# Kernel tuning notes

Measured on AMD Instinct MI355X. Metric: run time of the kernel, lower is better.

Reference implementation:

```python
import jax, jax.numpy as jnp
import numpy as np

B, S, F, L = 128, 512, 128, 1024  # batch, seq_len, n_features, latent_dim


def _gru_step(h, x, W_ih, W_hh, b_ih, b_hh):
    # PyTorch GRUCell math, gate order (r, z, n)
    gi = x @ W_ih.T + b_ih            # [B, 3L]
    gh = h @ W_hh.T + b_hh            # [B, 3L]
    ir, iz, inn = jnp.split(gi, 3, axis=-1)
    hr, hz, hn = jnp.split(gh, 3, axis=-1)
    r = jax.nn.sigmoid(ir + hr)
    z = jax.nn.sigmoid(iz + hz)
    n = jnp.tanh(inn + r * hn)
    return (1.0 - z) * n + z * h


def setup_inputs() -> dict:
    key = jax.random.key(0)
    ks = jax.random.split(key, 12)
    s_e = 1.0 / np.sqrt(L)
    u = lambda k, shape: jax.random.uniform(k, shape, jnp.float32, -s_e, s_e)
    return {
        "x": jax.random.normal(ks[0], (B, S, F), jnp.float32),
        # encoder GRU (single layer)
        "W_ih_e": u(ks[1], (3 * L, F)),
        "W_hh_e": u(ks[2], (3 * L, L)),
        "b_ih_e": u(ks[3], (3 * L,)),
        "b_hh_e": u(ks[4], (3 * L,)),
        # decoder GRUCell
        "W_ih_d": u(ks[5], (3 * L, F)),
        "W_hh_d": u(ks[6], (3 * L, L)),
        "b_ih_d": u(ks[7], (3 * L,)),
        "b_hh_d": u(ks[8], (3 * L,)),
        # decoder Linear(latent_dim -> n_features)
        "W_out": u(ks[9], (F, L)),
        "b_out": u(ks[10], (F,)),
    }


def reference(x, W_ih_e, W_hh_e, b_ih_e, b_hh_e,
              W_ih_d, W_hh_d, b_ih_d, b_hh_d, W_out, b_out):
    seq_len = x.shape[1]

    # ---- encoder: GRU over time, return final hidden state h_n [B, L] ----
    def enc_step(h, x_t):
        h = _gru_step(h, x_t, W_ih_e, W_hh_e, b_ih_e, b_hh_e)
        return h, None

    h0 = jnp.zeros((x.shape[0], W_hh_e.shape[1]), x.dtype)
    h_n, _ = jax.lax.scan(enc_step, h0, jnp.swapaxes(x, 0, 1))  # scan over [S,B,F]

    # ---- decoder: GRUCell + Linear unrolled seq_len steps ----
    x_init = h_n @ W_out.T + b_out  # [B, F]

    def dec_step(carry, _):
        h, x_i = carry
        h = _gru_step(h, x_i, W_ih_d, W_hh_d, b_ih_d, b_hh_d)
        x_i = h @ W_out.T + b_out
        return (h, x_i), x_i

    _, xs = jax.lax.scan(dec_step, (h_n, x_init), None, length=seq_len)  # [S,B,F]
    out = jnp.swapaxes(xs, 0, 1)  # [B,S,F]
    return jnp.flip(out, axis=1)
```

## Files before the change

kernel.cpp:

```cpp
#include <hip/hip_runtime.h>
#include <hip/hip_bf16.h>


#define B_ 128
#define S_ 512
#define F_ 128
#define L_ 1024
#define U_ 8
#define NWG_E 128
#define NWG_D 144

typedef __bf16 bf16x8 __attribute__((ext_vector_type(8)));
typedef float  f32x4  __attribute__((ext_vector_type(4)));
typedef float  f32x16 __attribute__((ext_vector_type(16)));
typedef int    i32x4  __attribute__((ext_vector_type(4)));
typedef unsigned long long u64;

union pk2 { unsigned u; __bf16 h[2]; };
union fu  { float f; unsigned u; };

#define MFMA32(a, b, c) __builtin_amdgcn_mfma_f32_32x32x16_bf16(a, b, c, 0, 0, 0)
#define Z16 f32x16{0.f,0.f,0.f,0.f,0.f,0.f,0.f,0.f,0.f,0.f,0.f,0.f,0.f,0.f,0.f,0.f}

#define LDG16(dst, p) asm volatile("global_load_dwordx4 %0, %1, off sc0 sc1" : "=v"(dst) : "v"(p))
#define VMWAIT16(a) asm volatile("s_waitcnt vmcnt(0)" \
    : "+v"(a[0]),"+v"(a[1]),"+v"(a[2]),"+v"(a[3]),"+v"(a[4]),"+v"(a[5]),"+v"(a[6]),"+v"(a[7]), \
      "+v"(a[8]),"+v"(a[9]),"+v"(a[10]),"+v"(a[11]),"+v"(a[12]),"+v"(a[13]),"+v"(a[14]),"+v"(a[15]) \
    :: "memory")
#define SB0() __builtin_amdgcn_sched_barrier(0)

#define O_H0   0
#define O_H1   (256*1024)
#define O_H32  (512*1024)
#define O_CTR  (1024*1024)
#define O_ZERO_END (1024*1024 + 8192)
#define O_XB   O_ZERO_END
#define O_WEH  (O_XB  + 16777216)
#define O_WEX  (O_WEH + 8388608)
#define O_BE   (O_WEX + 1048576)
#define O_WD   (O_BE  + 16384)
#define O_BD   (O_WD  + 8388608)
#define O_WC   (O_BD  + 16384)
#define O_WOB  (O_WC  + 6291456)


__global__ void k_xcvt(const float* __restrict__ x, __bf16* __restrict__ xb, int n) {
    int i = blockIdx.x * 256 + threadIdx.x;
    int stride = gridDim.x * 256;
    for (; i < n; i += stride) xb[i] = (__bf16)x[i];
}

__global__ void k_woutb(const float* __restrict__ Wout, __bf16* __restrict__ Wob, int n) {
    int i = blockIdx.x * 256 + threadIdx.x;
    if (i < n) Wob[i] = (__bf16)Wout[i];
}

__global__ void k_pack_enc(const float* __restrict__ Wih, const float* __restrict__ Whh,
                           const float* __restrict__ bih, const float* __restrict__ bhh,
                           __bf16* __restrict__ Weh, __bf16* __restrict__ Wex,
                           float* __restrict__ be) {
    int g = blockIdx.x, tid = threadIdx.x;
    for (int i = tid; i < 32 * 1024; i += 256) {
        int c = i >> 10, k = i & 1023;
        int u = g * U_ + (c >> 2), gate = c & 3;
        float v = 0.f;
        if (gate == 0)      v = Whh[(size_t)u * 1024 + k];
        else if (gate == 1) v = Whh[(size_t)(1024 + u) * 1024 + k];
        else if (gate == 3) v = Whh[(size_t)(2048 + u) * 1024 + k];
        Weh[((size_t)g * 32 + c) * 1024 + k] = (__bf16)v;
    }
    for (int i = tid; i < 32 * 128; i += 256) {
        int c = i >> 7, k = i & 127;
        int u = g * U_ + (c >> 2), gate = c & 3;
        float v = 0.f;
        if (gate == 0)      v = Wih[(size_t)u * 128 + k];
        else if (gate == 1) v = Wih[(size_t)(1024 + u) * 128 + k];
        else if (gate == 2) v = Wih[(size_t)(2048 + u) * 128 + k];
        Wex[((size_t)g * 32 + c) * 128 + k] = (__bf16)v;
    }
    if (tid < 32) {
        int c = tid, u = g * U_ + (c >> 2), gate = c & 3;
        float v;
        if (gate == 0)      v = bih[u] + bhh[u];
        else if (gate == 1) v = bih[1024 + u] + bhh[1024 + u];
        else if (gate == 2) v = bih[2048 + u];
        else                v = bhh[2048 + u];
        be[g * 32 + c] = v;
    }
}

__global__ void k_wcomb(const float* __restrict__ Wihd, const float* __restrict__ Wout,
                        __bf16* __restrict__ Wc) {
    __shared__ float a[8][128];
    int r0 = blockIdx.x * 8, tid = threadIdx.x;
    for (int i = tid; i < 8 * 128; i += 256)
        a[i >> 7][i & 127] = Wihd[(size_t)(r0 + (i >> 7)) * 128 + (i & 127)];
    __syncthreads();
    for (int j = tid; j < 1024; j += 256) {
        float acc[8] = {0, 0, 0, 0, 0, 0, 0, 0};
        for (int f = 0; f < 128; ++f) {
            float w = Wout[(size_t)f * 1024 + j];
#pragma unroll
            for (int r = 0; r < 8; ++r) acc[r] += a[r][f] * w;
        }
        for (int r = 0; r < 8; ++r) Wc[(size_t)(r0 + r) * 1024 + j] = (__bf16)acc[r];
    }
}

__global__ void k_pack_dec(const float* __restrict__ Whhd, const __bf16* __restrict__ Wc,
                           const float* __restrict__ Wihd,
                           const float* __restrict__ bihd, const float* __restrict__ bhhd,
                           const float* __restrict__ bout,
                           __bf16* __restrict__ Wd, float* __restrict__ bd) {
    int g = blockIdx.x, tid = threadIdx.x;
    for (int i = tid; i < 32 * 1024; i += 256) {
        int c = i >> 10, k = i & 1023;
        int u = g * U_ + (c >> 2), gate = c & 3;
        float v;
        if (gate == 0)      v = Whhd[(size_t)u * 1024 + k] + (float)Wc[(size_t)u * 1024 + k];
        else if (gate == 1) v = Whhd[(size_t)(1024 + u) * 1024 + k] + (float)Wc[(size_t)(1024 + u) * 1024 + k];
        else if (gate == 2) v = (float)Wc[(size_t)(2048 + u) * 1024 + k];
        else                v = Whhd[(size_t)(2048 + u) * 1024 + k];
        Wd[((size_t)g * 32 + c) * 1024 + k] = (__bf16)v;
    }
    if (tid < 32) {
        int c = tid;
        int u = g * U_ + (c >> 2), gate = c & 3;
        int row = (gate == 0) ? u : (gate == 1) ? (1024 + u) : (2048 + u);
        float v;
        if (gate <= 1) {
            float d = 0.f;
            for (int f = 0; f < 128; ++f) d += Wihd[(size_t)row * 128 + f] * bout[f];
            v = d + bihd[row] + bhhd[row];
        } else if (gate == 2) {
            float d = 0.f;
            for (int f = 0; f < 128; ++f) d += Wihd[(size_t)row * 128 + f] * bout[f];
            v = d + bihd[row];
        } else {
            v = bhhd[row];
        }
        bd[g * 32 + c] = v;
    }
}


__device__ __forceinline__ void bar_arrive(unsigned* base, int g) {
    if (threadIdx.x == 0)
        __hip_atomic_fetch_add(base + (g & 15) * 32, 1u,
                               __ATOMIC_RELAXED, __HIP_MEMORY_SCOPE_AGENT);
}

__device__ __forceinline__ void bar_wait(unsigned* base, unsigned tgt) {
    if (threadIdx.x == 0) {
        for (;;) {
            unsigned sum = 0;
#pragma unroll
            for (int j = 0; j < 16; ++j)
                sum += __hip_atomic_load(base + j * 32, __ATOMIC_RELAXED, __HIP_MEMORY_SCOPE_AGENT);
            if (sum >= tgt) break;
            __builtin_amdgcn_s_sleep(1);
        }
    }
    __syncthreads();
}

__global__ __launch_bounds__(512, 2) void k_enc(
    const __bf16* __restrict__ xb, const __bf16* __restrict__ Weh,
    const __bf16* __restrict__ Wex, const float* __restrict__ be,
    __bf16* __restrict__ h0, __bf16* __restrict__ h1,
    float* __restrict__ h32, unsigned* __restrict__ ctr) {
    __shared__ __align__(16) __bf16 sWh[32][1032];
    __shared__ __align__(16) __bf16 sWx[32][136];
    __shared__ float sB[32];
    __shared__ __align__(16) float sGa[128][36];
    __shared__ __align__(16) float sGb[128][36];
    const int g = blockIdx.x, tid = threadIdx.x;
    const int lane = tid & 63, wave = tid >> 6;

    for (int i = tid; i < 32 * 128; i += 512) {
        int c = i >> 7, k8 = i & 127;
        *(i32x4*)&sWh[c][k8 * 8] = *(const i32x4*)(Weh + ((size_t)g * 32 + c) * 1024 + k8 * 8);
    }
    for (int i = tid; i < 32 * 16; i += 512) {
        int c = i >> 4, k8 = i & 15;
        *(i32x4*)&sWx[c][k8 * 8] = *(const i32x4*)(Wex + ((size_t)g * 32 + c) * 128 + k8 * 8);
    }
    if (tid < 32) sB[tid] = be[g * 32 + tid];
    __syncthreads();

    const int bcol = lane & 31;
    const int koff = (lane >> 5) * 8;
    const int mrow = (wave & 3) * 32 + bcol;
    const int kb = (wave >> 2) * 32;
    const bool up = (wave >= 4);

    bf16x8 xrg[8];
    if (up) {
#pragma unroll
        for (int kt = 0; kt < 8; ++kt) xrg[kt] = *(const bf16x8*)(&sWx[bcol][kt * 16 + koff]);
    }

    const int erow = tid >> 2, pair = tid & 3;
    const int hidx2 = g * 512 + erow * 4 + pair;
    float ha = 0.f, hb = 0.f;

    f32x16 accx = Z16;
    if (up) {
        const __bf16* xr = xb + (size_t)mrow * 65536;
#pragma unroll
        for (int kt = 0; kt < 8; ++kt)
            accx = MFMA32(*(const bf16x8*)(xr + kt * 16 + koff), xrg[kt], accx);
    }

    for (int s = 0; s < 512; ++s) {
        const __bf16* hcur = (s & 1) ? h1 : h0;
        __bf16* hnxt = (s & 1) ? h0 : h1;
        {
            f32x16 aA = up ? accx : Z16;
            f32x16 aB = Z16;
            const __bf16* hr = hcur + ((size_t)(kb * 2 + (koff >> 3)) << 10) + mrow * 8;
            bf16x8 af[16];
#pragma unroll
            for (int i = 0; i < 16; ++i) LDG16(af[i], hr + i * 2048);
            VMWAIT16(af); SB0();
#pragma unroll
            for (int i = 0; i < 16; ++i) {
                const bf16x8 b = *(const bf16x8*)(&sWh[bcol][(kb + i) * 16 + koff]);
                if (i & 1) aB = MFMA32(af[i], b, aB); else aA = MFMA32(af[i], b, aA);
                LDG16(af[i], hr + (16 + i) * 2048);
            }
            VMWAIT16(af); SB0();
#pragma unroll
            for (int i = 0; i < 16; ++i) {
                const bf16x8 b = *(const bf16x8*)(&sWh[bcol][(kb + 16 + i) * 16 + koff]);
                if (i & 1) aB = MFMA32(af[i], b, aB); else aA = MFMA32(af[i], b, aA);
            }
            f32x16 acc = aA + aB;
            int rb = (wave & 3) * 32 + 4 * (lane >> 5);
            float (*sg)[36] = up ? sGb : sGa;
#pragma unroll
            for (int r = 0; r < 16; ++r)
                sg[rb + (r & 3) + 8 * (r >> 2)][bcol] = acc[r];
        }
        __syncthreads();
        {
            f32x4 g0 = *(const f32x4*)&sGa[erow][pair * 8] + *(const f32x4*)&sGb[erow][pair * 8];
            f32x4 g1 = *(const f32x4*)&sGa[erow][pair * 8 + 4] + *(const f32x4*)&sGb[erow][pair * 8 + 4];
            int c0 = pair * 8;
            float r = 1.f / (1.f + __expf(-(g0[0] + sB[c0 + 0])));
            float z = 1.f / (1.f + __expf(-(g0[1] + sB[c0 + 1])));
            float n = tanhf(g0[2] + sB[c0 + 2] + r * (g0[3] + sB[c0 + 3]));
            ha = (1.f - z) * n + z * ha;
            r = 1.f / (1.f + __expf(-(g1[0] + sB[c0 + 4])));
            z = 1.f / (1.f + __expf(-(g1[1] + sB[c0 + 5])));
            n = tanhf(g1[2] + sB[c0 + 6] + r * (g1[3] + sB[c0 + 7]));
            hb = (1.f - z) * n + z * hb;
            pk2 p; p.h[0] = (__bf16)ha; p.h[1] = (__bf16)hb;
            __hip_atomic_store((unsigned*)hnxt + hidx2, p.u, __ATOMIC_RELAXED, __HIP_MEMORY_SCOPE_AGENT);
            if (s == 511) {
                h32[erow * 1024 + g * 8 + pair * 2]     = ha;
                h32[erow * 1024 + g * 8 + pair * 2 + 1] = hb;
            }
        }
        if (s < 511) {
            __syncthreads();
            bar_arrive(ctr, g);
            if (up) {
                f32x16 ax = Z16;
                const __bf16* xr = xb + (size_t)mrow * 65536 + (size_t)(s + 1) * 128;
#pragma unroll
                for (int kt = 0; kt < 8; ++kt)
                    ax = MFMA32(*(const bf16x8*)(xr + kt * 16 + koff), xrg[kt], ax);
                accx = ax;
            }
            bar_wait(ctr, (unsigned)(s + 1) * NWG_E);
        }
    }
}

__global__ __launch_bounds__(512, 2) void k_dec(
    const __bf16* __restrict__ Wd, const float* __restrict__ bd,
    const __bf16* __restrict__ Wob, const float* __restrict__ bout,
    __bf16* __restrict__ h0, __bf16* __restrict__ h1,
    const float* __restrict__ h32, float* __restrict__ out,
    unsigned* __restrict__ ctr) {
    __shared__ __align__(16) __bf16 sW[32][1032];
    __shared__ float sB[32];
    __shared__ __align__(16) float sGa[128][36];
    __shared__ __align__(16) float sGb[128][36];
    const int g = blockIdx.x, tid = threadIdx.x;
    const int lane = tid & 63, wave = tid >> 6;
    const bool gwg = (g < 128);
    const int go = g - 128;

    if (gwg) {
        for (int i = tid; i < 32 * 128; i += 512) {
            int c = i >> 7, k8 = i & 127;
            *(i32x4*)&sW[c][k8 * 8] = *(const i32x4*)(Wd + ((size_t)g * 32 + c) * 1024 + k8 * 8);
        }
        if (tid < 32) sB[tid] = bd[g * 32 + tid];
    } else {
        for (int i = tid; i < 32 * 128; i += 512) {
            int c = i >> 7, k8 = i & 127;
            *(i32x4*)&sW[c][k8 * 8] =
                *(const i32x4*)(Wob + ((size_t)((go >> 2) * 32 + c)) * 1024 + k8 * 8);
        }
        if (tid < 32) sB[tid] = bout[(go >> 2) * 32 + tid];
    }
    __syncthreads();

    const int bcol = lane & 31;
    const int koff = (lane >> 5) * 8;
    const int kb = (wave >> 2) * 32;
    const bool up = (wave >= 4);
    const int arow = gwg ? ((wave & 3) * 32 + bcol)
                         : ((go & 3) * 32 + bcol);

    const int erow = tid >> 2, pair = tid & 3;
    const int hidx2 = g * 512 + erow * 4 + pair;
    float ha = 0.f, hb = 0.f;
    if (gwg) {
        ha = h32[erow * 1024 + g * 8 + pair * 2];
        hb = h32[erow * 1024 + g * 8 + pair * 2 + 1];
    }

    if (gwg) {
        for (int s = 0; s < 512; ++s) {
            const __bf16* hcur = (s & 1) ? h1 : h0;
            __bf16* hnxt = (s & 1) ? h0 : h1;
            {
                f32x16 aA = Z16, aB = Z16;
                const __bf16* hr = hcur + ((size_t)(kb * 2 + (koff >> 3)) << 10) + arow * 8;
                bf16x8 af[16];
#pragma unroll
                for (int i = 0; i < 16; ++i) LDG16(af[i], hr + i * 2048);
                VMWAIT16(af); SB0();
#pragma unroll
                for (int i = 0; i < 16; ++i) {
                    const bf16x8 b = *(const bf16x8*)(&sW[bcol][(kb + i) * 16 + koff]);
                    if (i & 1) aB = MFMA32(af[i], b, aB); else aA = MFMA32(af[i], b, aA);
                    LDG16(af[i], hr + (16 + i) * 2048);
                }
                VMWAIT16(af); SB0();
#pragma unroll
                for (int i = 0; i < 16; ++i) {
                    const bf16x8 b = *(const bf16x8*)(&sW[bcol][(kb + 16 + i) * 16 + koff]);
                    if (i & 1) aB = MFMA32(af[i], b, aB); else aA = MFMA32(af[i], b, aA);
                }
                f32x16 acc = aA + aB;
                int rb = (wave & 3) * 32 + 4 * (lane >> 5);
                float (*sg)[36] = up ? sGb : sGa;
#pragma unroll
                for (int r = 0; r < 16; ++r)
                    sg[rb + (r & 3) + 8 * (r >> 2)][bcol] = acc[r];
            }
            __syncthreads();
            {
                f32x4 g0 = *(const f32x4*)&sGa[erow][pair * 8] + *(const f32x4*)&sGb[erow][pair * 8];
                f32x4 g1 = *(const f32x4*)&sGa[erow][pair * 8 + 4] + *(const f32x4*)&sGb[erow][pair * 8 + 4];
                int c0 = pair * 8;
                float r = 1.f / (1.f + __expf(-(g0[0] + sB[c0 + 0])));
                float z = 1.f / (1.f + __expf(-(g0[1] + sB[c0 + 1])));
                float n = tanhf(g0[2] + sB[c0 + 2] + r * (g0[3] + sB[c0 + 3]));
                ha = (1.f - z) * n + z * ha;
                r = 1.f / (1.f + __expf(-(g1[0] + sB[c0 + 4])));
                z = 1.f / (1.f + __expf(-(g1[1] + sB[c0 + 5])));
                n = tanhf(g1[2] + sB[c0 + 6] + r * (g1[3] + sB[c0 + 7]));
                hb = (1.f - z) * n + z * hb;
                pk2 p; p.h[0] = (__bf16)ha; p.h[1] = (__bf16)hb;
                __hip_atomic_store((unsigned*)hnxt + hidx2, p.u, __ATOMIC_RELAXED, __HIP_MEMORY_SCOPE_AGENT);
            }
            __syncthreads();
            bar_arrive(ctr, g);
            if (s < 511) bar_wait(ctr, (unsigned)(s + 1) * NWG_D);
        }
    } else {
        __shared__ __align__(16) float sGo[4][32][32];
        for (int s = 0; s <= 512; ++s) {
            const __bf16* hcur = (s & 1) ? h1 : h0;
            const bool cmp = (wave < 4) && (s >= 1);
            if (cmp) {
                f32x16 aA = Z16, aB = Z16;
                const __bf16* hr = hcur + ((size_t)(wave * 32 + (koff >> 3)) << 10) + arow * 8;
                bf16x8 af[16];
#pragma unroll
                for (int i = 0; i < 16; ++i) LDG16(af[i], hr + i * 2048);
                VMWAIT16(af); SB0();
#pragma unroll
                for (int i = 0; i < 16; ++i) {
                    const bf16x8 b = *(const bf16x8*)(&sW[bcol][(wave * 16 + i) * 16 + koff]);
                    if (i & 1) aB = MFMA32(af[i], b, aB); else aA = MFMA32(af[i], b, aA);
                }
                f32x16 acc = aA + aB;
                int rb = 4 * (lane >> 5);
#pragma unroll
                for (int r = 0; r < 16; ++r)
                    sGo[wave][rb + (r & 3) + 8 * (r >> 2)][bcol] = acc[r];
            }
            __syncthreads();
            if (s < 512) bar_arrive(ctr, g);
            if (s >= 1) {
                int c = tid & 31, r0 = (tid >> 5) & 15;
#pragma unroll
                for (int hh = 0; hh < 2; ++hh) {
                    int r = r0 + hh * 16;
                    fu cv;
                    cv.f = sGo[0][r][c] + sGo[1][r][c] + sGo[2][r][c] + sGo[3][r][c] + sB[c];
                    size_t off = ((size_t)((go & 3) * 32 + r) * 512 + (size_t)(512 - s)) * 128
                               + (go >> 2) * 32 + c;
                    __hip_atomic_store((unsigned*)(out + off), cv.u,
                                       __ATOMIC_RELAXED, __HIP_MEMORY_SCOPE_AGENT);
                }
            }
            if (s < 512) bar_wait(ctr, (unsigned)(s + 1) * NWG_D);
        }
    }
}

extern "C" void kernel_launch(void* const* d_in, const int* in_sizes, int n_in,
                              void* d_out, int out_size, void* d_ws, size_t ws_size,
                              hipStream_t stream) {
    (void)in_sizes; (void)n_in; (void)out_size; (void)ws_size;
    const float* x    = (const float*)d_in[0];
    const float* Wihe = (const float*)d_in[1];
    const float* Whhe = (const float*)d_in[2];
    const float* bihe = (const float*)d_in[3];
    const float* bhhe = (const float*)d_in[4];
    const float* Wihd = (const float*)d_in[5];
    const float* Whhd = (const float*)d_in[6];
    const float* bihd = (const float*)d_in[7];
    const float* bhhd = (const float*)d_in[8];
    const float* Wout = (const float*)d_in[9];
    const float* bout = (const float*)d_in[10];

    char* ws = (char*)d_ws;
    __bf16*   h0  = (__bf16*)(ws + O_H0);
    __bf16*   h1  = (__bf16*)(ws + O_H1);
    float*    h32 = (float*)(ws + O_H32);
    unsigned* ctr = (unsigned*)(ws + O_CTR);
    __bf16*   xbf = (__bf16*)(ws + O_XB);
    __bf16*   Weh = (__bf16*)(ws + O_WEH);
    __bf16*   Wex = (__bf16*)(ws + O_WEX);
    float*    be  = (float*)(ws + O_BE);
    __bf16*   Wd  = (__bf16*)(ws + O_WD);
    float*    bd  = (float*)(ws + O_BD);
    __bf16*   Wc  = (__bf16*)(ws + O_WC);
    __bf16*   Wob = (__bf16*)(ws + O_WOB);

    hipMemsetAsync(ws, 0, O_ZERO_END, stream);

    k_xcvt<<<4096, 256, 0, stream>>>(x, xbf, B_ * S_ * F_);
    k_pack_enc<<<NWG_E, 256, 0, stream>>>(Wihe, Whhe, bihe, bhhe, Weh, Wex, be);
    k_wcomb<<<384, 256, 0, stream>>>(Wihd, Wout, Wc);
    k_pack_dec<<<NWG_E, 256, 0, stream>>>(Whhd, Wc, Wihd, bihd, bhhd, bout, Wd, bd);
    k_woutb<<<512, 256, 0, stream>>>(Wout, Wob, F_ * L_);

    k_enc<<<NWG_E, 512, 0, stream>>>(xbf, Weh, Wex, be, h0, h1, h32, ctr);
    k_dec<<<NWG_D, 512, 0, stream>>>(Wd, bd, Wob, bout, h0, h1, h32, (float*)d_out,
                                     ctr + 1024);
}
```

Baseline: 6.005 ms.

## Halve workgroup count with 64 gate columns per WG and register-resident weights

Each persistent workgroup now owns 16 hidden units (64 gate columns) instead of 8, so the encoder runs 64 WGs and the decoder 68 instead of 128/144. Half of each WG's recurrent weight slice is held in VGPRs and the other half in LDS. The x-projection is split across all waves, and the output WGs now each cover a full batch of 32 features with vectorized stores. The aim is to cut grid-barrier participants and per-step synchronization cost. In exchange, each WG does twice the MFMA work per step and carries much higher register pressure.

```diff
diff --git a/kernel.cpp b/kernel.cpp
--- a/kernel.cpp
+++ b/kernel.cpp
@@ -6,9 +6,8 @@
 #define S_ 512
 #define F_ 128
 #define L_ 1024
-#define U_ 8
-#define NWG_E 128
-#define NWG_D 144
+#define NWG_E 64
+#define NWG_D 68
 
 typedef __bf16 bf16x8 __attribute__((ext_vector_type(8)));
 typedef float  f32x4  __attribute__((ext_vector_type(4)));
@@ -17,7 +16,6 @@
 typedef unsigned long long u64;
 
 union pk2 { unsigned u; __bf16 h[2]; };
-union fu  { float f; unsigned u; };
 
 #define MFMA32(a, b, c) __builtin_amdgcn_mfma_f32_32x32x16_bf16(a, b, c, 0, 0, 0)
 #define Z16 f32x16{0.f,0.f,0.f,0.f,0.f,0.f,0.f,0.f,0.f,0.f,0.f,0.f,0.f,0.f,0.f,0.f}
@@ -60,32 +58,32 @@
                            __bf16* __restrict__ Weh, __bf16* __restrict__ Wex,
                            float* __restrict__ be) {
     int g = blockIdx.x, tid = threadIdx.x;
-    for (int i = tid; i < 32 * 1024; i += 256) {
+    for (int i = tid; i < 64 * 1024; i += 256) {
         int c = i >> 10, k = i & 1023;
-        int u = g * U_ + (c >> 2), gate = c & 3;
+        int u = g * 16 + (c >> 2), gate = c & 3;
         float v = 0.f;
         if (gate == 0)      v = Whh[(size_t)u * 1024 + k];
         else if (gate == 1) v = Whh[(size_t)(1024 + u) * 1024 + k];
         else if (gate == 3) v = Whh[(size_t)(2048 + u) * 1024 + k];
-        Weh[((size_t)g * 32 + c) * 1024 + k] = (__bf16)v;
-    }
-    for (int i = tid; i < 32 * 128; i += 256) {
+        Weh[((size_t)g * 64 + c) * 1024 + k] = (__bf16)v;
+    }
+    for (int i = tid; i < 64 * 128; i += 256) {
         int c = i >> 7, k = i & 127;
-        int u = g * U_ + (c >> 2), gate = c & 3;
+        int u = g * 16 + (c >> 2), gate = c & 3;
         float v = 0.f;
         if (gate == 0)      v = Wih[(size_t)u * 128 + k];
         else if (gate == 1) v = Wih[(size_t)(1024 + u) * 128 + k];
         else if (gate == 2) v = Wih[(size_t)(2048 + u) * 128 + k];
-        Wex[((size_t)g * 32 + c) * 128 + k] = (__bf16)v;
-    }
-    if (tid < 32) {
-        int c = tid, u = g * U_ + (c >> 2), gate = c & 3;
+        Wex[((size_t)g * 64 + c) * 128 + k] = (__bf16)v;
+    }
+    if (tid < 64) {
+        int c = tid, u = g * 16 + (c >> 2), gate = c & 3;
         float v;
         if (gate == 0)      v = bih[u] + bhh[u];
         else if (gate == 1) v = bih[1024 + u] + bhh[1024 + u];
         else if (gate == 2) v = bih[2048 + u];
         else                v = bhh[2048 + u];
-        be[g * 32 + c] = v;
+        be[g * 64 + c] = v;
     }
 }
 
@@ -113,19 +111,19 @@
                            const float* __restrict__ bout,
                            __bf16* __restrict__ Wd, float* __restrict__ bd) {
     int g = blockIdx.x, tid = threadIdx.x;
-    for (int i = tid; i < 32 * 1024; i += 256) {
+    for (int i = tid; i < 64 * 1024; i += 256) {
         int c = i >> 10, k = i & 1023;
-        int u = g * U_ + (c >> 2), gate = c & 3;
+        int u = g * 16 + (c >> 2), gate = c & 3;
         float v;
         if (gate == 0)      v = Whhd[(size_t)u * 1024 + k] + (float)Wc[(size_t)u * 1024 + k];
         else if (gate == 1) v = Whhd[(size_t)(1024 + u) * 1024 + k] + (float)Wc[(size_t)(1024 + u) * 1024 + k];
         else if (gate == 2) v = (float)Wc[(size_t)(2048 + u) * 1024 + k];
         else                v = Whhd[(size_t)(2048 + u) * 1024 + k];
-        Wd[((size_t)g * 32 + c) * 1024 + k] = (__bf16)v;
-    }
-    if (tid < 32) {
+        Wd[((size_t)g * 64 + c) * 1024 + k] = (__bf16)v;
+    }
+    if (tid < 64) {
         int c = tid;
-        int u = g * U_ + (c >> 2), gate = c & 3;
+        int u = g * 16 + (c >> 2), gate = c & 3;
         int row = (gate == 0) ? u : (gate == 1) ? (1024 + u) : (2048 + u);
         float v;
         if (gate <= 1) {
@@ -139,7 +137,7 @@
         } else {
             v = bhhd[row];
         }
-        bd[g * 32 + c] = v;
+        bd[g * 64 + c] = v;
     }
 }
 
@@ -169,109 +167,119 @@
     const __bf16* __restrict__ Wex, const float* __restrict__ be,
     __bf16* __restrict__ h0, __bf16* __restrict__ h1,
     float* __restrict__ h32, unsigned* __restrict__ ctr) {
-    __shared__ __align__(16) __bf16 sWh[32][1032];
-    __shared__ __align__(16) __bf16 sWx[32][136];
-    __shared__ float sB[32];
-    __shared__ __align__(16) float sGa[128][36];
-    __shared__ __align__(16) float sGb[128][36];
+    __shared__ __align__(16) __bf16 sWl[64][544];
+    __shared__ __align__(16) __bf16 sWx[64][136];
+    __shared__ __align__(16) float sB[64];
+    __shared__ __align__(16) float sG[2][128][68];
     const int g = blockIdx.x, tid = threadIdx.x;
     const int lane = tid & 63, wave = tid >> 6;
 
-    for (int i = tid; i < 32 * 128; i += 512) {
-        int c = i >> 7, k8 = i & 127;
-        *(i32x4*)&sWh[c][k8 * 8] = *(const i32x4*)(Weh + ((size_t)g * 32 + c) * 1024 + k8 * 8);
-    }
-    for (int i = tid; i < 32 * 16; i += 512) {
-        int c = i >> 4, k8 = i & 15;
-        *(i32x4*)&sWx[c][k8 * 8] = *(const i32x4*)(Wex + ((size_t)g * 32 + c) * 128 + k8 * 8);
-    }
-    if (tid < 32) sB[tid] = be[g * 32 + tid];
+    for (int i = tid; i < 64 * 64; i += 512) {
+        int c = i >> 6, q = i & 63;
+        int fp = q >> 1, half = q & 1;
+        int kf = (fp >> 4) * 32 + 16 + (fp & 15);
+        *(i32x4*)&sWl[c][q * 8] = *(const i32x4*)(Weh + ((size_t)g * 64 + c) * 1024 + kf * 16 + half * 8);
+    }
+    for (int i = tid; i < 64 * 16; i += 512) {
+        int c = i >> 4, q = i & 15;
+        *(i32x4*)&sWx[c][q * 8] = *(const i32x4*)(Wex + ((size_t)g * 64 + c) * 128 + q * 8);
+    }
+    if (tid < 64) sB[tid] = be[g * 64 + tid];
     __syncthreads();
 
     const int bcol = lane & 31;
     const int koff = (lane >> 5) * 8;
-    const int mrow = (wave & 3) * 32 + bcol;
-    const int kb = (wave >> 2) * 32;
-    const bool up = (wave >= 4);
-
-    bf16x8 xrg[8];
-    if (up) {
-#pragma unroll
-        for (int kt = 0; kt < 8; ++kt) xrg[kt] = *(const bf16x8*)(&sWx[bcol][kt * 16 + koff]);
-    }
-
-    const int erow = tid >> 2, pair = tid & 3;
-    const int hidx2 = g * 512 + erow * 4 + pair;
-    float ha = 0.f, hb = 0.f;
-
-    f32x16 accx = Z16;
-    if (up) {
-        const __bf16* xr = xb + (size_t)mrow * 65536;
-#pragma unroll
-        for (int kt = 0; kt < 8; ++kt)
-            accx = MFMA32(*(const bf16x8*)(xr + kt * 16 + koff), xrg[kt], accx);
+    const int rs = wave & 3, ks = wave >> 2;
+    const int arow = rs * 32 + bcol;
+
+    bf16x8 br0[16], br1[16];
+#pragma unroll
+    for (int i = 0; i < 16; ++i) {
+        int kf = ks * 32 + i;
+        br0[i] = *(const bf16x8*)(Weh + ((size_t)g * 64 + bcol) * 1024 + kf * 16 + koff);
+        br1[i] = *(const bf16x8*)(Weh + ((size_t)g * 64 + 32 + bcol) * 1024 + kf * 16 + koff);
+    }
+
+    const int erow = tid >> 2, p4 = tid & 3;
+    float hst[4] = {0.f, 0.f, 0.f, 0.f};
+
+    f32x16 ax0 = Z16, ax1 = Z16;
+    {
+        const __bf16* xr = xb + (size_t)arow * 65536;
+#pragma unroll
+        for (int i = 0; i < 4; ++i) {
+            int kf = ks * 4 + i;
+            bf16x8 a = *(const bf16x8*)(xr + kf * 16 + koff);
+            ax0 = MFMA32(a, *(const bf16x8*)(&sWx[bcol][kf * 16 + koff]), ax0);
+            ax1 = MFMA32(a, *(const bf16x8*)(&sWx[32 + bcol][kf * 16 + koff]), ax1);
+        }
     }
 
     for (int s = 0; s < 512; ++s) {
         const __bf16* hcur = (s & 1) ? h1 : h0;
         __bf16* hnxt = (s & 1) ? h0 : h1;
         {
-            f32x16 aA = up ? accx : Z16;
-            f32x16 aB = Z16;
-            const __bf16* hr = hcur + ((size_t)(kb * 2 + (koff >> 3)) << 10) + mrow * 8;
+            f32x16 a0 = ax0, a1 = ax1;
+            const __bf16* hr = hcur + ((size_t)(ks * 64 + (koff >> 3)) << 10) + arow * 8;
             bf16x8 af[16];
 #pragma unroll
             for (int i = 0; i < 16; ++i) LDG16(af[i], hr + i * 2048);
             VMWAIT16(af); SB0();
 #pragma unroll
             for (int i = 0; i < 16; ++i) {
-                const bf16x8 b = *(const bf16x8*)(&sWh[bcol][(kb + i) * 16 + koff]);
-                if (i & 1) aB = MFMA32(af[i], b, aB); else aA = MFMA32(af[i], b, aA);
+                a0 = MFMA32(af[i], br0[i], a0);
+                a1 = MFMA32(af[i], br1[i], a1);
                 LDG16(af[i], hr + (16 + i) * 2048);
             }
             VMWAIT16(af); SB0();
 #pragma unroll
             for (int i = 0; i < 16; ++i) {
-                const bf16x8 b = *(const bf16x8*)(&sWh[bcol][(kb + 16 + i) * 16 + koff]);
-                if (i & 1) aB = MFMA32(af[i], b, aB); else aA = MFMA32(af[i], b, aA);
-            }
-            f32x16 acc = aA + aB;
-            int rb = (wave & 3) * 32 + 4 * (lane >> 5);
-            float (*sg)[36] = up ? sGb : sGa;
-#pragma unroll
-            for (int r = 0; r < 16; ++r)
-                sg[rb + (r & 3) + 8 * (r >> 2)][bcol] = acc[r];
+                int fp = ks * 16 + i;
+                a0 = MFMA32(af[i], *(const bf16x8*)(&sWl[bcol][fp * 16 + koff]), a0);
+                a1 = MFMA32(af[i], *(const bf16x8*)(&sWl[32 + bcol][fp * 16 + koff]), a1);
+            }
+            int rb = rs * 32 + 4 * (lane >> 5);
+#pragma unroll
+            for (int r = 0; r < 16; ++r) {
+                int rw = rb + (r & 3) + 8 * (r >> 2);
+                sG[ks][rw][bcol] = a0[r];
+                sG[ks][rw][32 + bcol] = a1[r];
+            }
         }
         __syncthreads();
         {
-            f32x4 g0 = *(const f32x4*)&sGa[erow][pair * 8] + *(const f32x4*)&sGb[erow][pair * 8];
-            f32x4 g1 = *(const f32x4*)&sGa[erow][pair * 8 + 4] + *(const f32x4*)&sGb[erow][pair * 8 + 4];
-            int c0 = pair * 8;
-            float r = 1.f / (1.f + __expf(-(g0[0] + sB[c0 + 0])));
-            float z = 1.f / (1.f + __expf(-(g0[1] + sB[c0 + 1])));
-            float n = tanhf(g0[2] + sB[c0 + 2] + r * (g0[3] + sB[c0 + 3]));
-            ha = (1.f - z) * n + z * ha;
-            r = 1.f / (1.f + __expf(-(g1[0] + sB[c0 + 4])));
-            z = 1.f / (1.f + __expf(-(g1[1] + sB[c0 + 5])));
-            n = tanhf(g1[2] + sB[c0 + 6] + r * (g1[3] + sB[c0 + 7]));
-            hb = (1.f - z) * n + z * hb;
-            pk2 p; p.h[0] = (__bf16)ha; p.h[1] = (__bf16)hb;
-            __hip_atomic_store((unsigned*)hnxt + hidx2, p.u, __ATOMIC_RELAXED, __HIP_MEMORY_SCOPE_AGENT);
+#pragma unroll
+            for (int uu = 0; uu < 4; ++uu) {
+                int c0 = (p4 * 4 + uu) * 4;
+                f32x4 v = *(const f32x4*)&sG[0][erow][c0] + *(const f32x4*)&sG[1][erow][c0];
+                float r = 1.f / (1.f + __expf(-(v[0] + sB[c0 + 0])));
+                float z = 1.f / (1.f + __expf(-(v[1] + sB[c0 + 1])));
+                float n = tanhf(v[2] + sB[c0 + 2] + r * (v[3] + sB[c0 + 3]));
+                hst[uu] = (1.f - z) * n + z * hst[uu];
+            }
+#pragma unroll
+            for (int j = 0; j < 2; ++j) {
+                int lu = p4 * 4 + 2 * j;
+                pk2 p; p.h[0] = (__bf16)hst[2 * j]; p.h[1] = (__bf16)hst[2 * j + 1];
+                int hidx2 = (g * 2 + (lu >> 3)) * 512 + erow * 4 + ((lu >> 1) & 3);
+                __hip_atomic_store((unsigned*)hnxt + hidx2, p.u, __ATOMIC_RELAXED, __HIP_MEMORY_SCOPE_AGENT);
+            }
             if (s == 511) {
-                h32[erow * 1024 + g * 8 + pair * 2]     = ha;
-                h32[erow * 1024 + g * 8 + pair * 2 + 1] = hb;
+                f32x4 o; o[0] = hst[0]; o[1] = hst[1]; o[2] = hst[2]; o[3] = hst[3];
+                *(f32x4*)(h32 + erow * 1024 + g * 16 + p4 * 4) = o;
             }
         }
         if (s < 511) {
             __syncthreads();
             bar_arrive(ctr, g);
-            if (up) {
-                f32x16 ax = Z16;
-                const __bf16* xr = xb + (size_t)mrow * 65536 + (size_t)(s + 1) * 128;
-#pragma unroll
-                for (int kt = 0; kt < 8; ++kt)
-                    ax = MFMA32(*(const bf16x8*)(xr + kt * 16 + koff), xrg[kt], ax);
-                accx = ax;
+            ax0 = Z16; ax1 = Z16;
+            const __bf16* xr = xb + (size_t)arow * 65536 + (size_t)(s + 1) * 128;
+#pragma unroll
+            for (int i = 0; i < 4; ++i) {
+                int kf = ks * 4 + i;
+                bf16x8 a = *(const bf16x8*)(xr + kf * 16 + koff);
+                ax0 = MFMA32(a, *(const bf16x8*)(&sWx[bcol][kf * 16 + koff]), ax0);
+                ax1 = MFMA32(a, *(const bf16x8*)(&sWx[32 + bcol][kf * 16 + koff]), ax1);
             }
             bar_wait(ctr, (unsigned)(s + 1) * NWG_E);
         }
@@ -284,132 +292,152 @@
     __bf16* __restrict__ h0, __bf16* __restrict__ h1,
     const float* __restrict__ h32, float* __restrict__ out,
     unsigned* __restrict__ ctr) {
-    __shared__ __align__(16) __bf16 sW[32][1032];
-    __shared__ float sB[32];
-    __shared__ __align__(16) float sGa[128][36];
-    __shared__ __align__(16) float sGb[128][36];
+    __shared__ __align__(16) __bf16 sWl[64][544];
+    __shared__ __align__(16) float sB[64];
+    __shared__ __align__(16) float sG[2][128][68];
     const int g = blockIdx.x, tid = threadIdx.x;
     const int lane = tid & 63, wave = tid >> 6;
-    const bool gwg = (g < 128);
-    const int go = g - 128;
-
-    if (gwg) {
-        for (int i = tid; i < 32 * 128; i += 512) {
-            int c = i >> 7, k8 = i & 127;
-            *(i32x4*)&sW[c][k8 * 8] = *(const i32x4*)(Wd + ((size_t)g * 32 + c) * 1024 + k8 * 8);
-        }
-        if (tid < 32) sB[tid] = bd[g * 32 + tid];
-    } else {
-        for (int i = tid; i < 32 * 128; i += 512) {
-            int c = i >> 7, k8 = i & 127;
-            *(i32x4*)&sW[c][k8 * 8] =
-                *(const i32x4*)(Wob + ((size_t)((go >> 2) * 32 + c)) * 1024 + k8 * 8);
-        }
-        if (tid < 32) sB[tid] = bout[(go >> 2) * 32 + tid];
-    }
-    __syncthreads();
+    const bool gwg = (g < 64);
 
     const int bcol = lane & 31;
     const int koff = (lane >> 5) * 8;
-    const int kb = (wave >> 2) * 32;
-    const bool up = (wave >= 4);
-    const int arow = gwg ? ((wave & 3) * 32 + bcol)
-                         : ((go & 3) * 32 + bcol);
-
-    const int erow = tid >> 2, pair = tid & 3;
-    const int hidx2 = g * 512 + erow * 4 + pair;
-    float ha = 0.f, hb = 0.f;
+    const int rs = wave & 3, ks = wave >> 2;
+    const int arow = rs * 32 + bcol;
+
     if (gwg) {
-        ha = h32[erow * 1024 + g * 8 + pair * 2];
-        hb = h32[erow * 1024 + g * 8 + pair * 2 + 1];
-    }
-
-    if (gwg) {
+        for (int i = tid; i < 64 * 64; i += 512) {
+            int c = i >> 6, q = i & 63;
+            int fp = q >> 1, half = q & 1;
+            int kf = (fp >> 4) * 32 + 16 + (fp & 15);
+            *(i32x4*)&sWl[c][q * 8] = *(const i32x4*)(Wd + ((size_t)g * 64 + c) * 1024 + kf * 16 + half * 8);
+        }
+        if (tid < 64) sB[tid] = bd[g * 64 + tid];
+        __syncthreads();
+
+        bf16x8 br0[16], br1[16];
+#pragma unroll
+        for (int i = 0; i < 16; ++i) {
+            int kf = ks * 32 + i;
+            br0[i] = *(const bf16x8*)(Wd + ((size_t)g * 64 + bcol) * 1024 + kf * 16 + koff);
+            br1[i] = *(const bf16x8*)(Wd + ((size_t)g * 64 + 32 + bcol) * 1024 + kf * 16 + koff);
+        }
+
+        const int erow = tid >> 2, p4 = tid & 3;
+        float hst[4];
+        {
+            f32x4 hi = *(const f32x4*)(h32 + erow * 1024 + g * 16 + p4 * 4);
+            hst[0] = hi[0]; hst[1] = hi[1]; hst[2] = hi[2]; hst[3] = hi[3];
+        }
+
         for (int s = 0; s < 512; ++s) {
             const __bf16* hcur = (s & 1) ? h1 : h0;
             __bf16* hnxt = (s & 1) ? h0 : h1;
             {
-                f32x16 aA = Z16, aB = Z16;
-                const __bf16* hr = hcur + ((size_t)(kb * 2 + (koff >> 3)) << 10) + arow * 8;
+                f32x16 a0 = Z16, a1 = Z16;
+                const __bf16* hr = hcur + ((size_t)(ks * 64 + (koff >> 3)) << 10) + arow * 8;
                 bf16x8 af[16];
 #pragma unroll
                 for (int i = 0; i < 16; ++i) LDG16(af[i], hr + i * 2048);
                 VMWAIT16(af); SB0();
 #pragma unroll
                 for (int i = 0; i < 16; ++i) {
-                    const bf16x8 b = *(const bf16x8*)(&sW[bcol][(kb + i) * 16 + koff]);
-                    if (i & 1) aB = MFMA32(af[i], b, aB); else aA = MFMA32(af[i], b, aA);
+                    a0 = MFMA32(af[i], br0[i], a0);
+                    a1 = MFMA32(af[i], br1[i], a1);
                     LDG16(af[i], hr + (16 + i) * 2048);
                 }
                 VMWAIT16(af); SB0();
 #pragma unroll
                 for (int i = 0; i < 16; ++i) {
-                    const bf16x8 b = *(const bf16x8*)(&sW[bcol][(kb + 16 + i) * 16 + koff]);
-                    if (i & 1) aB = MFMA32(af[i], b, aB); else aA = MFMA32(af[i], b, aA);
-                }
-                f32x16 acc = aA + aB;
-                int rb = (wave & 3) * 32 + 4 * (lane >> 5);
-                float (*sg)[36] = up ? sGb : sGa;
-#pragma unroll
-                for (int r = 0; r < 16; ++r)
-                    sg[rb + (r & 3) + 8 * (r >> 2)][bcol] = acc[r];
+                    int fp = ks * 16 + i;
+                    a0 = MFMA32(af[i], *(const bf16x8*)(&sWl[bcol][fp * 16 + koff]), a0);
+                    a1 = MFMA32(af[i], *(const bf16x8*)(&sWl[32 + bcol][fp * 16 + koff]), a1);
+                }
+                int rb = rs * 32 + 4 * (lane >> 5);
+#pragma unroll
+                for (int r = 0; r < 16; ++r) {
+                    int rw = rb + (r & 3) + 8 * (r >> 2);
+                    sG[ks][rw][bcol] = a0[r];
+                    sG[ks][rw][32 + bcol] = a1[r];
+                }
             }
             __syncthreads();
             {
-                f32x4 g0 = *(const f32x4*)&sGa[erow][pair * 8] + *(const f32x4*)&sGb[erow][pair * 8];
-                f32x4 g1 = *(const f32x4*)&sGa[erow][pair * 8 + 4] + *(const f32x4*)&sGb[erow][pair * 8 + 4];
-                int c0 = pair * 8;
-                float r = 1.f / (1.f + __expf(-(g0[0] + sB[c0 + 0])));
-                float z = 1.f / (1.f + __expf(-(g0[1] + sB[c0 + 1])));
-                float n = tanhf(g0[2] + sB[c0 + 2] + r * (g0[3] + sB[c0 + 3]));
-                ha = (1.f - z) * n + z * ha;
-                r = 1.f / (1.f + __expf(-(g1[0] + sB[c0 + 4])));
-                z = 1.f / (1.f + __expf(-(g1[1] + sB[c0 + 5])));
-                n = tanhf(g1[2] + sB[c0 + 6] + r * (g1[3] + sB[c0 + 7]));
-                hb = (1.f - z) * n + z * hb;
-                pk2 p; p.h[0] = (__bf16)ha; p.h[1] = (__bf16)hb;
-                __hip_atomic_store((unsigned*)hnxt + hidx2, p.u, __ATOMIC_RELAXED, __HIP_MEMORY_SCOPE_AGENT);
+                const int erow2 = erow, p42 = p4;
+#pragma unroll
+                for (int uu = 0; uu < 4; ++uu) {
+                    int c0 = (p42 * 4 + uu) * 4;
+                    f32x4 v = *(const f32x4*)&sG[0][erow2][c0] + *(const f32x4*)&sG[1][erow2][c0];
+                    float r = 1.f / (1.f + __expf(-(v[0] + sB[c0 + 0])));
+                    float z = 1.f / (1.f + __expf(-(v[1] + sB[c0 + 1])));
+                    float n = tanhf(v[2] + sB[c0 + 2] + r * (v[3] + sB[c0 + 3]));
+                    hst[uu] = (1.f - z) * n + z * hst[uu];
+                }
+#pragma unroll
+                for (int j = 0; j < 2; ++j) {
+                    int lu = p42 * 4 + 2 * j;
+                    pk2 p; p.h[0] = (__bf16)hst[2 * j]; p.h[1] = (__bf16)hst[2 * j + 1];
+                    int hidx2 = (g * 2 + (lu >> 3)) * 512 + erow2 * 4 + ((lu >> 1) & 3);
+                    __hip_atomic_store((unsigned*)hnxt + hidx2, p.u, __ATOMIC_RELAXED, __HIP_MEMORY_SCOPE_AGENT);
+                }
             }
             __syncthreads();
             bar_arrive(ctr, g);
             if (s < 511) bar_wait(ctr, (unsigned)(s + 1) * NWG_D);
         }
     } else {
-        __shared__ __align__(16) float sGo[4][32][32];
+        const int go = g - 64;
+        const int fbase = go * 32;
+        for (int i = tid; i < 32 * 64; i += 512) {
+            int c = i >> 6, q = i & 63;
+            int fp = q >> 1, half = q & 1;
+            int kf = (fp >> 4) * 32 + 16 + (fp & 15);
+            *(i32x4*)&sWl[c][q * 8] = *(const i32x4*)(Wob + ((size_t)(fbase + c)) * 1024 + kf * 16 + half * 8);
+        }
+        if (tid < 32) sB[tid] = bout[fbase + tid];
+        __syncthreads();
+
+        bf16x8 br[16];
+#pragma unroll
+        for (int i = 0; i < 16; ++i) {
+            int kf = ks * 32 + i;
+            br[i] = *(const bf16x8*)(Wob + ((size_t)(fbase + bcol)) * 1024 + kf * 16 + koff);
+        }
+
         for (int s = 0; s <= 512; ++s) {
             const __bf16* hcur = (s & 1) ? h1 : h0;
-            const bool cmp = (wave < 4) && (s >= 1);
-            if (cmp) {
-                f32x16 aA = Z16, aB = Z16;
-                const __bf16* hr = hcur + ((size_t)(wave * 32 + (koff >> 3)) << 10) + arow * 8;
+            if (s >= 1) {
+                f32x16 a0 = Z16;
+                const __bf16* hr = hcur + ((size_t)(ks * 64 + (koff >> 3)) << 10) + arow * 8;
                 bf16x8 af[16];
 #pragma unroll
                 for (int i = 0; i < 16; ++i) LDG16(af[i], hr + i * 2048);
                 VMWAIT16(af); SB0();
 #pragma unroll
                 for (int i = 0; i < 16; ++i) {
-                    const bf16x8 b = *(const bf16x8*)(&sW[bcol][(wave * 16 + i) * 16 + koff]);
-                    if (i & 1) aB = MFMA32(af[i], b, aB); else aA = MFMA32(af[i], b, aA);
-                }
-                f32x16 acc = aA + aB;
-                int rb = 4 * (lane >> 5);
+                    a0 = MFMA32(af[i], br[i], a0);
+                    LDG16(af[i], hr + (16 + i) * 2048);
+                }
+                VMWAIT16(af); SB0();
+#pragma unroll
+                for (int i = 0; i < 16; ++i) {
+                    int fp = ks * 16 + i;
+                    a0 = MFMA32(af[i], *(const bf16x8*)(&sWl[bcol][fp * 16 + koff]), a0);
+                }
+                int rb = rs * 32 + 4 * (lane >> 5);
 #pragma unroll
                 for (int r = 0; r < 16; ++r)
-                    sGo[wave][rb + (r & 3) + 8 * (r >> 2)][bcol] = acc[r];
+                    sG[ks][rb + (r & 3) + 8 * (r >> 2)][bcol] = a0[r];
             }
             __syncthreads();
             if (s < 512) bar_arrive(ctr, g);
             if (s >= 1) {
-                int c = tid & 31, r0 = (tid >> 5) & 15;
-#pragma unroll
-                for (int hh = 0; hh < 2; ++hh) {
-                    int r = r0 + hh * 16;
-                    fu cv;
-                    cv.f = sGo[0][r][c] + sGo[1][r][c] + sGo[2][r][c] + sGo[3][r][c] + sB[c];
-                    size_t off = ((size_t)((go & 3) * 32 + r) * 512 + (size_t)(512 - s)) * 128
-                               + (go >> 2) * 32 + c;
-                    __hip_atomic_store((unsigned*)(out + off), cv.u,
-                                       __ATOMIC_RELAXED, __HIP_MEMORY_SCOPE_AGENT);
+                int row = tid >> 2, q = tid & 3;
+#pragma unroll
+                for (int part = 0; part < 2; ++part) {
+                    int c0 = q * 4 + part * 16;
+                    f32x4 v = *(const f32x4*)&sG[0][row][c0] + *(const f32x4*)&sG[1][row][c0]
+                            + *(const f32x4*)&sB[c0];
+                    *(f32x4*)(out + (size_t)row * 65536 + (size_t)(512 - s) * 128 + fbase + c0) = v;
                 }
             }
             if (s < 512) bar_wait(ctr, (unsigned)(s + 1) * NWG_D);
```

New measurement: 8.206 ms. +36.6%, slower.
